# Performance work log

Measured on AMD Instinct MI355X. Metric: run time of the kernel, lower is better.

## Reference

```python
import jax, jax.numpy as jnp
import numpy as np

K_SEM = 5          # max_semantic_edges
THRESH = 0.2       # semantic_threshold
NEG_INF = -1e30


def setup_inputs() -> dict:
    key = jax.random.key(0)
    k1, k2 = jax.random.split(key)
    message_embeddings = jax.random.normal(k1, (8192, 256), dtype=jnp.float32)
    edge_emb_table = jax.random.normal(k2, (2, 64), dtype=jnp.float32)
    return {"message_embeddings": message_embeddings, "edge_emb_table": edge_emb_table}


def reference(message_embeddings, edge_emb_table):
    N = message_embeddings.shape[0]

    # ---- temporal edges: for each i -> [i,i+1] then [i+1,i] (interleaved) ----
    i = jnp.arange(N - 1)
    fwd = jnp.stack([i, i + 1])            # [2, N-1]
    bwd = jnp.stack([i + 1, i])            # [2, N-1]
    temporal = jnp.stack([fwd, bwd], axis=2).reshape(2, -1)   # [2, 2(N-1)]
    n_temporal = 2 * (N - 1)

    # ---- semantic edges: per-row top-k over sim[i, :i] with threshold ----
    norm = jnp.sqrt(jnp.sum(message_embeddings * message_embeddings, axis=1, keepdims=True))
    emb_n = message_embeddings / jnp.maximum(norm, 1e-12)     # F.normalize(p=2)
    sim = emb_n @ emb_n.T                                      # [N, N]

    r = jnp.arange(N)[:, None]
    c = jnp.arange(N)[None, :]
    # zero out diagonal and adjacent (temporal) pairs, as the torch mask does
    sim = sim * (jnp.abs(r - c) > 1)
    # restrict candidates to j < i (strictly earlier messages)
    cand = jnp.where(c < r, sim, NEG_INF)                      # [N, N]

    vals, idxs = jax.lax.top_k(cand, K_SEM)                    # [N, K]
    sem_src = idxs.reshape(-1)                                 # [N*K]
    sem_dst = jnp.repeat(jnp.arange(N), K_SEM)                 # [N*K]
    sem_valid = (vals > THRESH).reshape(-1)                    # [N*K]

    # ---- assemble padded fixed-size edge set ----
    edge_index = jnp.concatenate([temporal, jnp.stack([sem_src, sem_dst])], axis=1)
    edge_types = jnp.concatenate(
        [jnp.zeros((n_temporal,), jnp.int32), jnp.ones((N * K_SEM,), jnp.int32)])
    valid = jnp.concatenate([jnp.ones((n_temporal,), bool), sem_valid])

    edge_attr = edge_emb_table[edge_types] * valid[:, None].astype(edge_emb_table.dtype)
    edge_index = jnp.where(valid[None, :], edge_index, -1)
    return edge_index, edge_attr, valid
```

## Files before the change

### kernel.cpp

```cpp
#include <hip/hip_runtime.h>

#define N_MSG 8192
#define DIM 256
#define KS 5
#define THRESH 0.2f
#define QSCALE 192.0f
#define FILT_I 6672
#define N_TEMPORAL (2*(N_MSG-1))
#define N_EDGES (N_TEMPORAL + N_MSG*KS)
#define ATTR_OFF (2*N_EDGES)
#define VALID_OFF (ATTR_OFF + N_EDGES*64)
#define BM 128
#define NTILE (N_MSG / BM)
#define NBLOCKS (NTILE*(NTILE+1)/2)
#define CAP 32

typedef int   i32x4 __attribute__((ext_vector_type(4)));
typedef float f32x4 __attribute__((ext_vector_type(4)));

__device__ __forceinline__ void ins5(float v, int j, float (&vv)[KS], int (&xx)[KS]) {
    float cv = v; int cj = j;
#pragma unroll
    for (int k = 0; k < KS; ++k) {
        bool b = (cv > vv[k]) || (cv == vv[k] && cj < xx[k]);
        float tv = b ? vv[k] : cv; int tj = b ? xx[k] : cj;
        vv[k] = b ? cv : vv[k];    xx[k] = b ? cj : xx[k];
        cv = tv; cj = tj;
    }
}

__global__ void normalize_k(const float* __restrict__ emb, float* __restrict__ embn,
                            unsigned int* __restrict__ embqT, int* __restrict__ cnt) {
    int lane = threadIdx.x & 63;
    int row = blockIdx.x * 4 + (threadIdx.x >> 6);
    const float4 x = *(const float4*)(emb + (size_t)row * DIM + lane * 4);
    float ss = x.x * x.x;
    ss = fmaf(x.y, x.y, ss); ss = fmaf(x.z, x.z, ss); ss = fmaf(x.w, x.w, ss);
#pragma unroll
    for (int off = 1; off <= 32; off <<= 1) ss += __shfl_xor(ss, off);
    float nrm = fmaxf(sqrtf(ss), 1e-12f);
    f32x4 y; y.x = x.x / nrm; y.y = x.y / nrm; y.z = x.z / nrm; y.w = x.w / nrm;
    __builtin_nontemporal_store(y, (f32x4*)(embn + (size_t)row * DIM + lane * 4));
    int q0 = (int)rintf(fminf(fmaxf(y.x * QSCALE, -127.f), 127.f));
    int q1 = (int)rintf(fminf(fmaxf(y.y * QSCALE, -127.f), 127.f));
    int q2 = (int)rintf(fminf(fmaxf(y.z * QSCALE, -127.f), 127.f));
    int q3 = (int)rintf(fminf(fmaxf(y.w * QSCALE, -127.f), 127.f));
    unsigned int packed =
        (q0 & 255) | ((q1 & 255) << 8) | ((q2 & 255) << 16) | ((q3 & 255) << 24);
    __builtin_nontemporal_store(packed,
        &embqT[(((size_t)(lane >> 2) * N_MSG + row) << 2) | (lane & 3)]);
    if (lane == 0) cnt[row] = 0;
}

__global__ __launch_bounds__(256, 4)
void sim_filter_k(const i32x4* __restrict__ T, int* __restrict__ cnt,
                  int* __restrict__ cidx) {
    int t = blockIdx.x;
    int bi = (int)((sqrtf(8.0f * (float)t + 1.0f) - 1.0f) * 0.5f);
    while ((bi + 1) * (bi + 2) / 2 <= t) ++bi;
    while (bi * (bi + 1) / 2 > t) --bi;
    int bj = t - bi * (bi + 1) / 2;
    const int i0 = bi * BM, j0 = bj * BM;

    const int tid = threadIdx.x;
    const int lane = tid & 63;
    const int ws = tid >> 6;
    const int wm = ws >> 1, wn = ws & 1;
    const int lr = lane & 15, kb = lane >> 4;

    i32x4 acc[4][4];
#pragma unroll
    for (int m = 0; m < 4; ++m)
#pragma unroll
        for (int n = 0; n < 4; ++n) { i32x4 z = {0, 0, 0, 0}; acc[m][n] = z; }

#pragma unroll
    for (int kc = 0; kc < 4; ++kc) {
        const i32x4* Tc = T + (size_t)(kc * 4 + kb) * N_MSG;
        i32x4 a[4], b[4];
#pragma unroll
        for (int f = 0; f < 4; ++f) {
            a[f] = Tc[i0 + wm * 64 + f * 16 + lr];
            b[f] = Tc[j0 + wn * 64 + f * 16 + lr];
        }
#pragma unroll
        for (int m = 0; m < 4; ++m)
#pragma unroll
            for (int n = 0; n < 4; ++n)
                acc[m][n] = __builtin_amdgcn_mfma_i32_16x16x64_i8(a[m], b[n], acc[m][n], 0, 0, 0);
    }

#pragma unroll
    for (int m = 0; m < 4; ++m) {
        int i = i0 + wm * 64 + m * 16 + kb * 4;
#pragma unroll
        for (int n = 0; n < 4; ++n) {
            int j = j0 + wn * 64 + n * 16 + lr;
#pragma unroll
            for (int r = 0; r < 4; ++r) {
                int v = acc[m][n][r];
                int ii = i + r;
                if (v > FILT_I && j <= ii - 2) {
                    int c = atomicAdd(&cnt[ii], 1);
                    if (c < CAP) cidx[(size_t)ii * CAP + c] = j;
                }
            }
        }
    }
}

template<bool FUSE>
__global__ void rescue_k(const float* __restrict__ embn, const int* __restrict__ cnt,
                         const int* __restrict__ cidx, const float* __restrict__ table,
                         float* __restrict__ out) {
    int lane = threadIdx.x & 63;
    int i = blockIdx.x * 4 + (threadIdx.x >> 6);
    int nc = cnt[i]; if (nc > CAP) nc = CAP;

    float fv[KS]; int fx[KS];
#pragma unroll
    for (int k = 0; k < KS; ++k) { fv[k] = -1e30f; fx[k] = -1; }

    if (nc > 0) {
        const float4 a = *(const float4*)(embn + (size_t)i * DIM + lane * 4);
        for (int c = 0; c < nc; ++c) {
            int j = cidx[(size_t)i * CAP + c];
            const float4 b = *(const float4*)(embn + (size_t)j * DIM + lane * 4);
            float p = a.x * b.x;
            p = fmaf(a.y, b.y, p); p = fmaf(a.z, b.z, p); p = fmaf(a.w, b.w, p);
#pragma unroll
            for (int off = 1; off <= 32; off <<= 1) p += __shfl_xor(p, off);
            if (p > THRESH) ins5(p, j, fv, fx);
        }
    }
    int vcnt = 0;
#pragma unroll
    for (int k = 0; k < KS; ++k) vcnt += (fv[k] > THRESH) ? 1 : 0;

    float tsem = FUSE ? table[64 + lane] : 0.0f;
#pragma unroll
    for (int k = 0; k < KS; ++k) {
        int e = N_TEMPORAL + i * KS + k;
        bool val = (k < vcnt);
        if (lane == 0) {
            out[e]             = val ? (float)fx[k] : -1.0f;
            out[N_EDGES + e]   = val ? (float)i     : -1.0f;
            out[VALID_OFF + e] = val ? 1.0f : 0.0f;
        }
        if (FUSE) out[ATTR_OFF + (size_t)e * 64 + lane] = val ? tsem : 0.0f;
    }
    if (FUSE) {
        if (i < N_MSG - 1) {
            float ttem = table[lane];
            int e0 = 2 * i;
            out[ATTR_OFF + (size_t)e0 * 64 + lane]       = ttem;
            out[ATTR_OFF + (size_t)(e0 + 1) * 64 + lane] = ttem;
            if (lane == 0) {
                out[e0]                 = (float)i;
                out[N_EDGES + e0]       = (float)(i + 1);
                out[VALID_OFF + e0]     = 1.0f;
                out[e0 + 1]             = (float)(i + 1);
                out[N_EDGES + e0 + 1]   = (float)i;
                out[VALID_OFF + e0 + 1] = 1.0f;
            }
        }
    }
}

__global__ void attr_out_k(const float* __restrict__ table, float* __restrict__ out) {
    int idx = blockIdx.x * 256 + threadIdx.x;
    int e = idx >> 4, sub = idx & 15;
    if (e >= N_EDGES) return;
    float4 a4;
    if (e < N_TEMPORAL) {
        a4 = *(const float4*)(table + sub * 4);
        if (sub == 0) {
            int i = e >> 1;
            out[e]             = (e & 1) ? (float)(i + 1) : (float)i;
            out[N_EDGES + e]   = (e & 1) ? (float)i       : (float)(i + 1);
            out[VALID_OFF + e] = 1.0f;
        }
    } else {
        float vld = out[VALID_OFF + e];
        a4 = *(const float4*)(table + 64 + sub * 4);
        a4.x *= vld; a4.y *= vld; a4.z *= vld; a4.w *= vld;
    }
    *(float4*)(out + ATTR_OFF + (size_t)e * 64 + sub * 4) = a4;
}

extern "C" void kernel_launch(void* const* d_in, const int* in_sizes, int n_in,
                              void* d_out, int out_size, void* d_ws, size_t ws_size,
                              hipStream_t stream) {
    const float* emb   = (const float*)d_in[0];
    const float* table = (const float*)d_in[1];
    float* out = (float*)d_out;

    size_t embn_f  = (size_t)N_MSG * DIM;
    size_t embq_f  = (size_t)N_MSG * DIM / 4;
    size_t cidx_f  = (size_t)N_MSG * CAP;
    size_t cnt_f   = N_MSG;
    size_t need_bytes = (embn_f + embq_f + cidx_f + cnt_f) * 4;

    bool have_ws = (ws_size >= need_bytes);
    float* scratch = have_ws ? (float*)d_ws
                             : out + ATTR_OFF;
    float*        embn  = scratch;
    unsigned int* embqT = (unsigned int*)(scratch + embn_f);
    int*          cidx  = (int*)(scratch + embn_f + embq_f);
    int*          cnt   = (int*)(scratch + embn_f + embq_f + cidx_f);

    normalize_k<<<N_MSG / 4, 256, 0, stream>>>(emb, embn, embqT, cnt);
    sim_filter_k<<<NBLOCKS, 256, 0, stream>>>((const i32x4*)embqT, cnt, cidx);
    if (have_ws) {
        rescue_k<true><<<N_MSG / 4, 256, 0, stream>>>(embn, cnt, cidx, table, out);
    } else {
        rescue_k<false><<<N_MSG / 4, 256, 0, stream>>>(embn, cnt, cidx, table, out);
        attr_out_k<<<((size_t)N_EDGES * 16 + 255) / 256, 256, 0, stream>>>(table, out);
    }
}
```

Measured before the change: 63.40 us.

## Retile similarity filter into 256x128 blocks with per-wave 64x128 strips

Changes the int8 MFMA similarity tiling from 128x128 triangular blocks, where each wave owns a 64x64 quadrant, to 256-row by 128-column blocks where each wave owns a 64x128 strip. Waves whose strip lies wholly above the causal diagonal exit early, which trims wasted work near the diagonal at a finer granularity. The block index mapping is rewritten for the new triangular layout, and launch bounds drop to 2 blocks per CU to allow the doubled accumulator count, at the cost of lower occupancy.

```diff
diff --git a/kernel.cpp b/kernel.cpp
--- a/kernel.cpp
+++ b/kernel.cpp
@@ -10,9 +10,8 @@
 #define N_EDGES (N_TEMPORAL + N_MSG*KS)
 #define ATTR_OFF (2*N_EDGES)
 #define VALID_OFF (ATTR_OFF + N_EDGES*64)
-#define BM 128
-#define NTILE (N_MSG / BM)
-#define NBLOCKS (NTILE*(NTILE+1)/2)
+#define NTI (N_MSG / 256)
+#define NBLOCKS (NTI * (NTI + 1))
 #define CAP 32
 
 typedef int   i32x4 __attribute__((ext_vector_type(4)));
@@ -52,50 +51,50 @@
     if (lane == 0) cnt[row] = 0;
 }
 
-__global__ __launch_bounds__(256, 4)
+__global__ __launch_bounds__(256, 2)
 void sim_filter_k(const i32x4* __restrict__ T, int* __restrict__ cnt,
                   int* __restrict__ cidx) {
     int t = blockIdx.x;
-    int bi = (int)((sqrtf(8.0f * (float)t + 1.0f) - 1.0f) * 0.5f);
-    while ((bi + 1) * (bi + 2) / 2 <= t) ++bi;
-    while (bi * (bi + 1) / 2 > t) --bi;
-    int bj = t - bi * (bi + 1) / 2;
-    const int i0 = bi * BM, j0 = bj * BM;
+    int I = (int)((sqrtf(4.0f * (float)t + 1.0f) - 1.0f) * 0.5f);
+    while ((I + 1) * (I + 2) <= t) ++I;
+    while (I * (I + 1) > t) --I;
+    int J = t - I * (I + 1);
 
     const int tid = threadIdx.x;
     const int lane = tid & 63;
-    const int ws = tid >> 6;
-    const int wm = ws >> 1, wn = ws & 1;
+    const int i0 = I * 256 + (tid >> 6) * 64;
+    const int j0 = J * 128;
+    if (j0 > i0 + 61) return;
+
     const int lr = lane & 15, kb = lane >> 4;
 
-    i32x4 acc[4][4];
+    i32x4 acc[4][8];
 #pragma unroll
     for (int m = 0; m < 4; ++m)
 #pragma unroll
-        for (int n = 0; n < 4; ++n) { i32x4 z = {0, 0, 0, 0}; acc[m][n] = z; }
+        for (int n = 0; n < 8; ++n) { i32x4 z = {0, 0, 0, 0}; acc[m][n] = z; }
 
 #pragma unroll
     for (int kc = 0; kc < 4; ++kc) {
         const i32x4* Tc = T + (size_t)(kc * 4 + kb) * N_MSG;
-        i32x4 a[4], b[4];
-#pragma unroll
-        for (int f = 0; f < 4; ++f) {
-            a[f] = Tc[i0 + wm * 64 + f * 16 + lr];
-            b[f] = Tc[j0 + wn * 64 + f * 16 + lr];
-        }
+        i32x4 a[4], b[8];
+#pragma unroll
+        for (int f = 0; f < 4; ++f) a[f] = Tc[i0 + f * 16 + lr];
+#pragma unroll
+        for (int g = 0; g < 8; ++g) b[g] = Tc[j0 + g * 16 + lr];
 #pragma unroll
         for (int m = 0; m < 4; ++m)
 #pragma unroll
-            for (int n = 0; n < 4; ++n)
+            for (int n = 0; n < 8; ++n)
                 acc[m][n] = __builtin_amdgcn_mfma_i32_16x16x64_i8(a[m], b[n], acc[m][n], 0, 0, 0);
     }
 
 #pragma unroll
     for (int m = 0; m < 4; ++m) {
-        int i = i0 + wm * 64 + m * 16 + kb * 4;
-#pragma unroll
-        for (int n = 0; n < 4; ++n) {
-            int j = j0 + wn * 64 + n * 16 + lr;
+        int i = i0 + m * 16 + kb * 4;
+#pragma unroll
+        for (int n = 0; n < 8; ++n) {
+            int j = j0 + n * 16 + lr;
 #pragma unroll
             for (int r = 0; r < 4; ++r) {
                 int v = acc[m][n][r];
```

After: 75.65 us. 19.3% more time.
